# Optimization experiments

Measured on AMD Instinct MI355X. Metric: run time of the kernel, lower is better.

The kernel has to match this reference:

```python
import jax, jax.numpy as jnp
import numpy as np

B, S, D, H, FF, R, NB = 8, 1024, 768, 12, 3072, 16, 768


def _ln(x, g, b, eps=1e-6):
    m = x.mean(-1, keepdims=True)
    v = jnp.mean((x - m) ** 2, axis=-1, keepdims=True)
    return (x - m) * jax.lax.rsqrt(v + eps) * g + b


def setup_inputs() -> dict:
    key = jax.random.key(0)

    def rn(i, shape, s=0.02):
        return jax.random.normal(jax.random.fold_in(key, i), shape, jnp.float32) * s

    inp = {
        "x": jax.random.normal(jax.random.fold_in(key, 0), (B, S, D), jnp.float32),
        "attn_mask": jnp.zeros((S, S), jnp.float32),
        "norm1_g": jnp.ones((D,), jnp.float32),
        "norm1_b": jnp.zeros((D,), jnp.float32),
        "q_w": rn(1, (D, D)), "q_b": jnp.zeros((D,), jnp.float32),
        "k_w": rn(2, (D, D)), "k_b": jnp.zeros((D,), jnp.float32),
        "v_w": rn(3, (D, D)), "v_b": jnp.zeros((D,), jnp.float32),
        "o_w": rn(4, (D, D)), "o_b": jnp.zeros((D,), jnp.float32),
        "norm2_g": jnp.ones((D,), jnp.float32),
        "norm2_b": jnp.zeros((D,), jnp.float32),
        "fc1_w": rn(5, (FF, D)), "fc1_b": jnp.zeros((FF,), jnp.float32),
        "fc2_w": rn(6, (D, FF)), "fc2_b": jnp.zeros((D,), jnp.float32),
        # shared LoRA (backbone tokens)
        "lora1_A": rn(7, (D, R)), "lora1_B": rn(8, (R, FF)),
        "lora2_A": rn(9, (FF, R)), "lora2_B": rn(10, (R, D)),
        # expert VeRA: frozen shared A/B, per-expert diagonal scaling vectors
        "vera1_A": rn(11, (D, R)), "vera1_B": rn(12, (R, FF)),
        "vera2_A": rn(13, (FF, R)), "vera2_B": rn(14, (R, D)),
        "expert_fc1_d": rn(15, (R,), 1.0), "expert_fc1_b": rn(16, (FF,), 1.0),
        "expert_fc2_d": rn(17, (R,), 1.0), "expert_fc2_b": rn(18, (D,), 1.0),
        "num_backbone_tokens": NB,
    }
    return inp


def reference(x, attn_mask, norm1_g, norm1_b, q_w, q_b, k_w, k_b, v_w, v_b,
              o_w, o_b, norm2_g, norm2_b, fc1_w, fc1_b, fc2_w, fc2_b,
              lora1_A, lora1_B, lora2_A, lora2_B,
              vera1_A, vera1_B, vera2_A, vera2_B,
              expert_fc1_d, expert_fc1_b, expert_fc2_d, expert_fc2_b,
              num_backbone_tokens):
    bsz, seq, dim = x.shape
    hd = dim // H                      # head_dim = 64
    scale = hd ** -0.5
    nb = num_backbone_tokens

    # ---- attention (manual bmm + mask + softmax, eval-mode dropout = identity) ----
    h = _ln(x, norm1_g, norm1_b)
    q = (h @ q_w.T + q_b).reshape(bsz, seq, H, hd)
    k = (h @ k_w.T + k_b).reshape(bsz, seq, H, hd)
    v = (h @ v_w.T + v_b).reshape(bsz, seq, H, hd)
    scores = jnp.einsum('bqhd,bkhd->bhqk', q * scale, k) + attn_mask  # [B,H,S,S]
    probs = jax.nn.softmax(scores, axis=-1)
    ao = jnp.einsum('bhqk,bkhd->bqhd', probs, v).reshape(bsz, seq, dim)
    x = x + (ao @ o_w.T + o_b)

    # ---- MLP with split backbone (shared LoRA) / expert (VeRA) adapters ----
    residual = x
    n2 = _ln(x, norm2_g, norm2_b)
    hid = n2 @ fc1_w.T + fc1_b                                   # [B,S,FF]
    hid_b = hid[:, :nb] + (n2[:, :nb] @ lora1_A) @ lora1_B
    hid_e = hid[:, nb:] + (((n2[:, nb:] @ vera1_A) * expert_fc1_d) @ vera1_B) * expert_fc1_b
    hid = jnp.concatenate([hid_b, hid_e], axis=1)
    hid = jax.nn.gelu(hid)
    out = hid @ fc2_w.T + fc2_b                                  # [B,S,D]
    out_b = out[:, :nb] + (hid[:, :nb] @ lora2_A) @ lora2_B
    out_e = out[:, nb:] + (((hid[:, nb:] @ vera2_A) * expert_fc2_d) @ vera2_B) * expert_fc2_b
    out = jnp.concatenate([out_b, out_e], axis=1)
    return residual + out
```

## Files before the change

kernel.cpp:

```cpp
#include <hip/hip_runtime.h>
#include <stdint.h>

#define B_  8
#define S_  1024
#define D_  768
#define H_  12
#define HD_ 64
#define FF_ 3072
#define M_  (B_*S_)
#define R_  16
#define QLD 2304

typedef unsigned short u16;
typedef short s16x8 __attribute__((ext_vector_type(8)));
typedef float fx4  __attribute__((ext_vector_type(4)));

__device__ __forceinline__ float b2f(u16 u) {
  union { unsigned int i; float f; } c; c.i = ((unsigned int)u) << 16; return c.f;
}
__device__ __forceinline__ u16 f2b(float f) {
  union { float f; unsigned int i; } c; c.f = f;
  unsigned int x = c.i;
  x += 0x7FFFu + ((x >> 16) & 1u);
  return (u16)(x >> 16);
}
__device__ __forceinline__ float gelu_f(float x) {
  float u = 0.7978845608028654f * (x + 0.044715f * x * x * x);
  float e = __expf(2.f * u);
  float t = 1.f - 2.f / (e + 1.f);
  return 0.5f * x * (1.f + t);
}
__device__ __forceinline__ void gload16(const u16* gsrc, u16* ldst) {
  __builtin_amdgcn_global_load_lds(
      (__attribute__((address_space(1))) void*)(gsrc),
      (__attribute__((address_space(3))) void*)(ldst), 16, 0, 0);
}

__global__ __launch_bounds__(256)
void cvt_f2b(const float* __restrict__ in, u16* __restrict__ out, int n4) {
  const int i = blockIdx.x * 256 + threadIdx.x;
  if (i < n4) {
    const float4 f = ((const float4*)in)[i];
    ushort4 o4; o4.x = f2b(f.x); o4.y = f2b(f.y); o4.z = f2b(f.z); o4.w = f2b(f.w);
    ((ushort4*)out)[i] = o4;
  }
}

__global__ __launch_bounds__(256)
void prep_qkvb(const float* qb, const float* kb, const float* vb, float* out) {
  const int i = blockIdx.x * 256 + threadIdx.x;
  if (i < QLD) out[i] = (i < D_) ? qb[i] : (i < 2 * D_) ? kb[i - D_] : vb[i - 2 * D_];
}
__global__ __launch_bounds__(256)
void prep_up(const float* __restrict__ Blora, const float* __restrict__ Bvera,
             const float* __restrict__ evec, u16* __restrict__ upL,
             u16* __restrict__ upV, int N) {
  const int f = blockIdx.x * 256 + threadIdx.x;
  if (f >= N) return;
  const float ev = evec[f];
  #pragma unroll
  for (int r = 0; r < 16; ++r) {
    upL[(size_t)f * 32 + r] = f2b(Blora[(size_t)r * N + f]);
    upV[(size_t)f * 32 + r] = f2b(Bvera[(size_t)r * N + f] * ev);
    upL[(size_t)f * 32 + 16 + r] = 0;
    upV[(size_t)f * 32 + 16 + r] = 0;
  }
}
__global__ __launch_bounds__(256)
void prep_a2t(const float* __restrict__ Alora, const float* __restrict__ Avera,
              u16* __restrict__ tL, u16* __restrict__ tV) {
  const int f = blockIdx.x * 256 + threadIdx.x;
  if (f >= FF_) return;
  const float4* apl = (const float4*)(Alora + (size_t)f * 16);
  const float4* apv = (const float4*)(Avera + (size_t)f * 16);
  #pragma unroll
  for (int q4 = 0; q4 < 4; ++q4) {
    const float4 l4 = apl[q4], v4 = apv[q4];
    tL[(size_t)(q4 * 4 + 0) * FF_ + f] = f2b(l4.x);
    tL[(size_t)(q4 * 4 + 1) * FF_ + f] = f2b(l4.y);
    tL[(size_t)(q4 * 4 + 2) * FF_ + f] = f2b(l4.z);
    tL[(size_t)(q4 * 4 + 3) * FF_ + f] = f2b(l4.w);
    tV[(size_t)(q4 * 4 + 0) * FF_ + f] = f2b(v4.x);
    tV[(size_t)(q4 * 4 + 1) * FF_ + f] = f2b(v4.y);
    tV[(size_t)(q4 * 4 + 2) * FF_ + f] = f2b(v4.z);
    tV[(size_t)(q4 * 4 + 3) * FF_ + f] = f2b(v4.w);
  }
}

template<bool ADD>
__global__ __launch_bounds__(256)
void ln_k(const float* __restrict__ x, const u16* __restrict__ add,
          const float* __restrict__ g, const float* __restrict__ beta,
          u16* __restrict__ outb, float* __restrict__ xsum,
          const float* __restrict__ Alora, const float* __restrict__ Avera,
          const float* __restrict__ dvec, u16* __restrict__ tmp1b,
          const int* __restrict__ nbp)
{
  const int row = blockIdx.x;
  const size_t base = (size_t)row * D_;
  float v0[3]; float s = 0.f, sq = 0.f;
  #pragma unroll
  for (int i = 0; i < 3; ++i) {
    const int d = threadIdx.x + i * 256;
    float val = x[base + d];
    if (ADD) { val += b2f(add[base + d]); xsum[base + d] = val; }
    v0[i] = val; s += val; sq += val * val;
  }
  #pragma unroll
  for (int mm = 32; mm >= 1; mm >>= 1) { s += __shfl_xor(s, mm); sq += __shfl_xor(sq, mm); }
  __shared__ float ss[4], s2[4];
  if ((threadIdx.x & 63) == 0) { ss[threadIdx.x >> 6] = s; s2[threadIdx.x >> 6] = sq; }
  __syncthreads();
  s  = ss[0] + ss[1] + ss[2] + ss[3];
  sq = s2[0] + s2[1] + s2[2] + s2[3];
  const float mean = s * (1.f / D_);
  const float var  = sq * (1.f / D_) - mean * mean;
  const float rs   = rsqrtf(var + 1e-6f);
  float nv[3];
  #pragma unroll
  for (int i = 0; i < 3; ++i) {
    const int d = threadIdx.x + i * 256;
    nv[i] = (v0[i] - mean) * rs * g[d] + beta[d];
    outb[base + d] = f2b(nv[i]);
  }

  if (ADD) {
    const int nb = *nbp;
    const bool ex = (row % S_) >= nb;
    const float* Am = ex ? Avera : Alora;
    float p[16];
    #pragma unroll
    for (int r = 0; r < 16; ++r) p[r] = 0.f;
    #pragma unroll
    for (int i = 0; i < 3; ++i) {
      const int d = threadIdx.x + i * 256;
      const float4* ap = (const float4*)(Am + (size_t)d * R_);
      const float4 a0 = ap[0], a1 = ap[1], a2 = ap[2], a3 = ap[3];
      const float vv = nv[i];
      p[0]  += vv * a0.x; p[1]  += vv * a0.y; p[2]  += vv * a0.z; p[3]  += vv * a0.w;
      p[4]  += vv * a1.x; p[5]  += vv * a1.y; p[6]  += vv * a1.z; p[7]  += vv * a1.w;
      p[8]  += vv * a2.x; p[9]  += vv * a2.y; p[10] += vv * a2.z; p[11] += vv * a2.w;
      p[12] += vv * a3.x; p[13] += vv * a3.y; p[14] += vv * a3.z; p[15] += vv * a3.w;
    }
    #pragma unroll
    for (int st = 1; st < 16; st <<= 1)
      #pragma unroll
      for (int r = 0; r < 16; ++r) p[r] += __shfl_xor(p[r], st);
    __shared__ float sred[16][16];
    const int grp = threadIdx.x >> 4;
    if ((threadIdx.x & 15) == 0) {
      #pragma unroll
      for (int r = 0; r < 16; ++r) sred[grp][r] = p[r];
    }
    __syncthreads();
    if (threadIdx.x < 16) {
      float v = 0.f;
      #pragma unroll
      for (int gg = 0; gg < 16; ++gg) v += sred[gg][threadIdx.x];
      if (ex) v *= dvec[threadIdx.x];
      tmp1b[(size_t)row * 32 + threadIdx.x] = f2b(v);
      tmp1b[(size_t)row * 32 + 16 + threadIdx.x] = 0;
    }
  }
}

template<int MODE>
__global__ __launch_bounds__(256)
void gemm_bt(const u16* __restrict__ A, const u16* __restrict__ W,
             const float* __restrict__ bias, u16* __restrict__ Cb,
             float* __restrict__ Cf, const float* __restrict__ resid,
             const u16* __restrict__ Aad, const u16* __restrict__ BadL,
             const u16* __restrict__ BadV, const int* __restrict__ nbp,
             int M, int N, int K)
{
  __shared__ u16 As[128 * 32];
  __shared__ u16 Bs[128 * 32];
  const int tid   = threadIdx.x;
  const int lane  = tid & 63;
  const int wid   = tid >> 6;
  const int wr    = wid >> 1;
  const int wc    = wid & 1;
  const int lr    = lane & 15;
  const int lk    = (lane >> 4) << 3;
  const int m0    = blockIdx.x * 128;
  const int n0    = blockIdx.y * 128;
  const int kg    = (tid & 3) * 8;
  const int row_a = tid >> 2;

  fx4 acc[4][4];
  const fx4 zero = {0.f, 0.f, 0.f, 0.f};
  #pragma unroll
  for (int i = 0; i < 4; ++i)
    #pragma unroll
    for (int j = 0; j < 4; ++j) acc[i][j] = zero;

  for (int k0 = 0; k0 < K; k0 += 32) {
    #pragma unroll
    for (int u = 0; u < 2; ++u) {
      const int row = u * 64 + row_a;
      const int li  = u * 256 + tid;
      gload16(A + (size_t)(m0 + row) * K + k0 + kg, &As[li * 8]);
      gload16(W + (size_t)(n0 + row) * K + k0 + kg, &Bs[li * 8]);
    }
    __syncthreads();
    s16x8 av[4], bv[4];
    #pragma unroll
    for (int i = 0; i < 4; ++i)
      av[i] = *(const s16x8*)&As[(wr * 64 + i * 16 + lr) * 32 + lk];
    #pragma unroll
    for (int j = 0; j < 4; ++j)
      bv[j] = *(const s16x8*)&Bs[(wc * 64 + j * 16 + lr) * 32 + lk];
    #pragma unroll
    for (int i = 0; i < 4; ++i)
      #pragma unroll
      for (int j = 0; j < 4; ++j)
        acc[i][j] = __builtin_amdgcn_mfma_f32_16x16x32_bf16(av[i], bv[j], acc[i][j], 0, 0, 0);
    __syncthreads();
  }

  if (MODE >= 1) {
    const int nb = *nbp;
    const u16* Bad = ((m0 % S_) >= nb) ? BadV : BadL;
    #pragma unroll
    for (int u = 0; u < 2; ++u) {
      const int row = u * 64 + row_a;
      const int li  = u * 256 + tid;
      gload16(Aad + (size_t)(m0 + row) * 32 + kg, &As[li * 8]);
      gload16(Bad + (size_t)(n0 + row) * 32 + kg, &Bs[li * 8]);
    }
    __syncthreads();
    s16x8 av[4], bv[4];
    #pragma unroll
    for (int i = 0; i < 4; ++i)
      av[i] = *(const s16x8*)&As[(wr * 64 + i * 16 + lr) * 32 + lk];
    #pragma unroll
    for (int j = 0; j < 4; ++j)
      bv[j] = *(const s16x8*)&Bs[(wc * 64 + j * 16 + lr) * 32 + lk];
    #pragma unroll
    for (int i = 0; i < 4; ++i)
      #pragma unroll
      for (int j = 0; j < 4; ++j)
        acc[i][j] = __builtin_amdgcn_mfma_f32_16x16x32_bf16(av[i], bv[j], acc[i][j], 0, 0, 0);
    __syncthreads();
  }

  const int rb = (lane >> 4) * 4;
  #pragma unroll
  for (int j = 0; j < 4; ++j) {
    const int col = n0 + wc * 64 + j * 16 + lr;
    const float bj = bias ? bias[col] : 0.f;
    #pragma unroll
    for (int i = 0; i < 4; ++i) {
      const int row = m0 + wr * 64 + i * 16 + rb;
      #pragma unroll
      for (int r = 0; r < 4; ++r) {
        const float val = acc[i][j][r] + bj;
        const size_t idx = (size_t)(row + r) * N + col;
        if (MODE == 1)      Cb[idx] = f2b(gelu_f(val));
        else if (MODE == 2) Cf[idx] = resid[idx] + val;
        else                Cb[idx] = f2b(val);
      }
    }
  }
}

__global__ __launch_bounds__(256)
void downproj(const u16* __restrict__ hid, const u16* __restrict__ A2tL,
              const u16* __restrict__ A2tV, float* __restrict__ part,
              const int* __restrict__ nbp)
{
  __shared__ u16 As[128 * 32];
  __shared__ u16 Bs[16 * 32];
  const int tid  = threadIdx.x;
  const int lane = tid & 63;
  const int w    = tid >> 6;
  const int lr   = lane & 15;
  const int lk   = (lane >> 4) << 3;
  const int m0   = blockIdx.x * 128;
  const int kb   = blockIdx.y * (FF_ / 8);
  const int nb   = *nbp;
  const u16* A2t = ((m0 % S_) >= nb) ? A2tV : A2tL;
  const int kg    = (tid & 3) * 8;
  const int row_a = tid >> 2;

  const fx4 zero = {0.f, 0.f, 0.f, 0.f};
  fx4 acc[2]; acc[0] = zero; acc[1] = zero;

  for (int k0 = kb; k0 < kb + FF_ / 8; k0 += 32) {
    #pragma unroll
    for (int u = 0; u < 2; ++u)
      gload16(hid + (size_t)(m0 + u * 64 + row_a) * FF_ + k0 + kg,
              &As[(u * 256 + tid) * 8]);
    if (tid < 64)
      gload16(A2t + (size_t)(tid >> 2) * FF_ + k0 + kg, &Bs[tid * 8]);
    __syncthreads();
    s16x8 bv = *(const s16x8*)&Bs[lr * 32 + lk];
    #pragma unroll
    for (int i = 0; i < 2; ++i) {
      s16x8 av = *(const s16x8*)&As[(w * 32 + i * 16 + lr) * 32 + lk];
      acc[i] = __builtin_amdgcn_mfma_f32_16x16x32_bf16(av, bv, acc[i], 0, 0, 0);
    }
    __syncthreads();
  }

  const int rb = (lane >> 4) * 4;
  #pragma unroll
  for (int i = 0; i < 2; ++i)
    #pragma unroll
    for (int r = 0; r < 4; ++r)
      part[(size_t)blockIdx.y * M_ * 16 +
           (size_t)(m0 + w * 32 + i * 16 + rb + r) * 16 + lr] = acc[i][r];
}

__global__ __launch_bounds__(256)
void reduce_dp(const float* __restrict__ part, const float* __restrict__ d2,
               u16* __restrict__ tmp2b, const int* __restrict__ nbp)
{
  const int idx = blockIdx.x * 256 + threadIdx.x;
  const int m = idx >> 4, r = idx & 15;
  const int nb = *nbp;
  float s = 0.f;
  #pragma unroll
  for (int ks = 0; ks < 8; ++ks) s += part[(size_t)ks * M_ * 16 + idx];
  if ((m % S_) >= nb) s *= d2[r];
  tmp2b[(size_t)m * 32 + r] = f2b(s);
  tmp2b[(size_t)m * 32 + 16 + r] = 0;
}

__global__ __launch_bounds__(256)
void attn_mfma(const u16* __restrict__ qkv, const float* __restrict__ mask,
               u16* __restrict__ o)
{
  __shared__ u16 Ql[64 * 64];
  __shared__ u16 Kl[64 * 64];
  __shared__ u16 Vt[64 * 64];
  __shared__ u16 Pl[4][16 * 64];

  const int tid  = threadIdx.x;
  const int lane = tid & 63;
  const int wq   = tid >> 6;
  const int lr   = lane & 15;
  const int hi   = lane >> 4;
  const int qb   = blockIdx.x;
  const int bh   = blockIdx.y;
  const int b    = bh / H_;
  const int h    = bh % H_;
  const size_t tok0 = (size_t)b * S_ + (size_t)qb * 64;
  const size_t colh = (size_t)h * HD_;

  #pragma unroll
  for (int u = 0; u < 2; ++u) {
    const int li = u * 256 + tid;
    const int r  = li >> 3;
    const int cb = ((li & 7) ^ (r & 7)) * 8;
    gload16(qkv + (tok0 + r) * QLD + colh + cb, &Ql[li * 8]);
  }
  __syncthreads();

  s16x8 qa[2];
  {
    const int qrow = wq * 16 + lr;
    #pragma unroll
    for (int ks = 0; ks < 2; ++ks)
      qa[ks] = *(const s16x8*)&Ql[qrow * 64 + ((ks * 32 + hi * 8) ^ ((qrow & 7) << 3))];
  }

  const fx4 zero = {0.f, 0.f, 0.f, 0.f};
  fx4 oacc[4];
  #pragma unroll
  for (int dj = 0; dj < 4; ++dj) oacc[dj] = zero;
  float mreg[4], lreg[4];
  #pragma unroll
  for (int r = 0; r < 4; ++r) { mreg[r] = -3.0e38f; lreg[r] = 0.f; }

  for (int kt = 0; kt < S_ / 64; ++kt) {
    const size_t ktok = (size_t)b * S_ + (size_t)kt * 64;
    __syncthreads();

    #pragma unroll
    for (int u = 0; u < 2; ++u) {
      const int li = u * 256 + tid;
      const int r  = li >> 3;
      const int cb = ((li & 7) ^ (r & 7)) * 8;
      gload16(qkv + (ktok + r) * QLD + D_ + colh + cb, &Kl[li * 8]);
    }
    {
      const int a  = tid >> 3;
      const int c8 = (tid & 7) * 8;
      const u16* vp = qkv + (ktok + 2 * a) * QLD + 2 * D_ + colh + c8;
      s16x8 v0 = *(const s16x8*)vp;
      s16x8 v1 = *(const s16x8*)(vp + QLD);
      #pragma unroll
      for (int jj = 0; jj < 8; ++jj) {
        const int d  = c8 + jj;
        const int sw = ((d & 7) ^ ((d >> 3) & 7)) << 3;
        const int cp = (2 * a) ^ sw;
        *(uint32_t*)&Vt[d * 64 + cp] =
            (uint32_t)(u16)v0[jj] | ((uint32_t)(u16)v1[jj] << 16);
      }
    }
    __syncthreads();

    float mv[4][4];
    {
      const float* mp = mask + (size_t)(qb * 64 + wq * 16 + hi * 4) * S_ + (size_t)kt * 64 + lr;
      #pragma unroll
      for (int r = 0; r < 4; ++r)
        #pragma unroll
        for (int j = 0; j < 4; ++j)
          mv[j][r] = mp[(size_t)r * S_ + j * 16];
    }

    s16x8 kb2[4][2];
    #pragma unroll
    for (int j = 0; j < 4; ++j) {
      const int n = j * 16 + lr;
      #pragma unroll
      for (int ks = 0; ks < 2; ++ks)
        kb2[j][ks] = *(const s16x8*)&Kl[n * 64 + ((ks * 32 + hi * 8) ^ ((n & 7) << 3))];
    }
    fx4 sf[4];
    #pragma unroll
    for (int j = 0; j < 4; ++j) sf[j] = zero;
    #pragma unroll
    for (int ks = 0; ks < 2; ++ks)
      #pragma unroll
      for (int j = 0; j < 4; ++j)
        sf[j] = __builtin_amdgcn_mfma_f32_16x16x32_bf16(qa[ks], kb2[j][ks], sf[j], 0, 0, 0);

    float val[4][4];
    #pragma unroll
    for (int j = 0; j < 4; ++j)
      #pragma unroll
      for (int r = 0; r < 4; ++r)
        val[j][r] = sf[j][r] * 0.125f + mv[j][r];
    #pragma unroll
    for (int r = 0; r < 4; ++r) {
      float mx = fmaxf(fmaxf(val[0][r], val[1][r]), fmaxf(val[2][r], val[3][r]));
      mx = fmaxf(mx, __shfl_xor(mx, 1));
      mx = fmaxf(mx, __shfl_xor(mx, 2));
      mx = fmaxf(mx, __shfl_xor(mx, 4));
      mx = fmaxf(mx, __shfl_xor(mx, 8));
      const float mn  = fmaxf(mreg[r], mx);
      const float fac = __expf(mreg[r] - mn);
      mreg[r] = mn;
      float rs = 0.f;
      #pragma unroll
      for (int j = 0; j < 4; ++j) {
        const float p = __expf(val[j][r] - mn);
        val[j][r] = p;
        rs += p;
      }
      rs += __shfl_xor(rs, 1); rs += __shfl_xor(rs, 2);
      rs += __shfl_xor(rs, 4); rs += __shfl_xor(rs, 8);
      lreg[r] = lreg[r] * fac + rs;
      #pragma unroll
      for (int dj = 0; dj < 4; ++dj) oacc[dj][r] *= fac;
    }

    #pragma unroll
    for (int j = 0; j < 4; ++j) {
      const int col = j * 16 + lr;
      #pragma unroll
      for (int r = 0; r < 4; ++r) {
        const int row = hi * 4 + r;
        Pl[wq][row * 64 + (col ^ ((row & 7) << 3))] = f2b(val[j][r]);
      }
    }
    s16x8 pa[2];
    #pragma unroll
    for (int ks = 0; ks < 2; ++ks)
      pa[ks] = *(const s16x8*)&Pl[wq][lr * 64 + ((ks * 32 + hi * 8) ^ ((lr & 7) << 3))];

    s16x8 bv2[4][2];
    #pragma unroll
    for (int dj = 0; dj < 4; ++dj) {
      const int n  = dj * 16 + lr;
      const int sw = ((n & 7) ^ ((n >> 3) & 7)) << 3;
      #pragma unroll
      for (int ks = 0; ks < 2; ++ks)
        bv2[dj][ks] = *(const s16x8*)&Vt[n * 64 + ((ks * 32 + hi * 8) ^ sw)];
    }
    #pragma unroll
    for (int ks = 0; ks < 2; ++ks)
      #pragma unroll
      for (int dj = 0; dj < 4; ++dj)
        oacc[dj] = __builtin_amdgcn_mfma_f32_16x16x32_bf16(pa[ks], bv2[dj][ks], oacc[dj], 0, 0, 0);
  }

  #pragma unroll
  for (int r = 0; r < 4; ++r) {
    const float inv = 1.f / lreg[r];
    const size_t grow = (tok0 + wq * 16 + hi * 4 + r) * D_ + colh;
    #pragma unroll
    for (int dj = 0; dj < 4; ++dj)
      o[grow + dj * 16 + lr] = f2b(oacc[dj][r] * inv);
  }
}

extern "C" void kernel_launch(void* const* d_in, const int* in_sizes, int n_in,
                              void* d_out, int out_size, void* d_ws, size_t ws_size,
                              hipStream_t stream)
{
  const float* x      = (const float*)d_in[0];
  const float* mask   = (const float*)d_in[1];
  const float* n1g    = (const float*)d_in[2];
  const float* n1b    = (const float*)d_in[3];
  const float* q_w    = (const float*)d_in[4];
  const float* q_bv   = (const float*)d_in[5];
  const float* k_w    = (const float*)d_in[6];
  const float* k_bv   = (const float*)d_in[7];
  const float* v_w    = (const float*)d_in[8];
  const float* v_bv   = (const float*)d_in[9];
  const float* o_w    = (const float*)d_in[10];
  const float* o_bv   = (const float*)d_in[11];
  const float* n2g    = (const float*)d_in[12];
  const float* n2b    = (const float*)d_in[13];
  const float* fc1_w  = (const float*)d_in[14];
  const float* fc1_bv = (const float*)d_in[15];
  const float* fc2_w  = (const float*)d_in[16];
  const float* fc2_bv = (const float*)d_in[17];
  const float* lora1A = (const float*)d_in[18];
  const float* lora1B = (const float*)d_in[19];
  const float* lora2A = (const float*)d_in[20];
  const float* lora2B = (const float*)d_in[21];
  const float* vera1A = (const float*)d_in[22];
  const float* vera1B = (const float*)d_in[23];
  const float* vera2A = (const float*)d_in[24];
  const float* vera2B = (const float*)d_in[25];
  const float* e1d    = (const float*)d_in[26];
  const float* e1b    = (const float*)d_in[27];
  const float* e2d    = (const float*)d_in[28];
  const float* e2b    = (const float*)d_in[29];
  const int*   nbp    = (const int*)d_in[30];

  char* wsb = (char*)d_ws;
  u16* h1    = (u16*)wsb; wsb += (size_t)M_ * D_ * 2;
  u16* qkv   = (u16*)wsb; wsb += (size_t)M_ * QLD * 2;
  u16* attno = (u16*)wsb; wsb += (size_t)M_ * D_ * 2;
  u16* oproj = (u16*)wsb; wsb += (size_t)M_ * D_ * 2;
  u16* n2    = (u16*)wsb; wsb += (size_t)M_ * D_ * 2;
  u16* wqkv  = (u16*)wsb; wsb += (size_t)QLD * D_ * 2;
  u16* wo    = (u16*)wsb; wsb += (size_t)D_ * D_ * 2;
  u16* wfc1  = (u16*)wsb; wsb += (size_t)FF_ * D_ * 2;
  u16* wfc2  = (u16*)wsb; wsb += (size_t)D_ * FF_ * 2;
  u16* tmp1b = (u16*)wsb; wsb += (size_t)M_ * 32 * 2;
  u16* tmp2b = (u16*)wsb; wsb += (size_t)M_ * 32 * 2;
  u16* up1L  = (u16*)wsb; wsb += (size_t)FF_ * 32 * 2;
  u16* up1V  = (u16*)wsb; wsb += (size_t)FF_ * 32 * 2;
  u16* up2L  = (u16*)wsb; wsb += (size_t)D_ * 32 * 2;
  u16* up2V  = (u16*)wsb; wsb += (size_t)D_ * 32 * 2;
  u16* a2tL  = (u16*)wsb; wsb += (size_t)16 * FF_ * 2;
  u16* a2tV  = (u16*)wsb; wsb += (size_t)16 * FF_ * 2;
  float* qkvb = (float*)wsb; wsb += (size_t)QLD * 4;
  float* part = (float*)wsb; wsb += (size_t)8 * M_ * 16 * 4;
  u16* hidb = h1;

  cvt_f2b<<<(D_*D_/4 + 255)/256, 256, 0, stream>>>(q_w, wqkv,              D_*D_/4);
  cvt_f2b<<<(D_*D_/4 + 255)/256, 256, 0, stream>>>(k_w, wqkv +   D_*D_,    D_*D_/4);
  cvt_f2b<<<(D_*D_/4 + 255)/256, 256, 0, stream>>>(v_w, wqkv + 2*D_*D_,    D_*D_/4);
  cvt_f2b<<<(D_*D_/4 + 255)/256, 256, 0, stream>>>(o_w,   wo,   D_*D_/4);
  cvt_f2b<<<(FF_*D_/4 + 255)/256, 256, 0, stream>>>(fc1_w, wfc1, FF_*D_/4);
  cvt_f2b<<<(D_*FF_/4 + 255)/256, 256, 0, stream>>>(fc2_w, wfc2, D_*FF_/4);
  prep_qkvb<<<(QLD + 255)/256, 256, 0, stream>>>(q_bv, k_bv, v_bv, qkvb);
  prep_up<<<(FF_ + 255)/256, 256, 0, stream>>>(lora1B, vera1B, e1b, up1L, up1V, FF_);
  prep_up<<<(D_  + 255)/256, 256, 0, stream>>>(lora2B, vera2B, e2b, up2L, up2V, D_);
  prep_a2t<<<(FF_ + 255)/256, 256, 0, stream>>>(lora2A, vera2A, a2tL, a2tV);

  ln_k<false><<<M_, 256, 0, stream>>>(x, nullptr, n1g, n1b, h1, nullptr,
                                      nullptr, nullptr, nullptr, nullptr, nullptr);
  gemm_bt<0><<<dim3(M_/128, QLD/128), 256, 0, stream>>>(
      h1, wqkv, qkvb, qkv, nullptr, nullptr, nullptr, nullptr, nullptr, nullptr,
      M_, QLD, D_);
  attn_mfma<<<dim3(S_/64, B_*H_), 256, 0, stream>>>(qkv, mask, attno);
  gemm_bt<0><<<dim3(M_/128, D_/128), 256, 0, stream>>>(
      attno, wo, o_bv, oproj, nullptr, nullptr, nullptr, nullptr, nullptr, nullptr,
      M_, D_, D_);

  ln_k<true><<<M_, 256, 0, stream>>>(x, oproj, n2g, n2b, n2, (float*)d_out,
                                     lora1A, vera1A, e1d, tmp1b, nbp);

  gemm_bt<1><<<dim3(M_/128, FF_/128), 256, 0, stream>>>(
      n2, wfc1, fc1_bv, hidb, nullptr, nullptr, tmp1b, up1L, up1V, nbp,
      M_, FF_, D_);

  downproj<<<dim3(M_/128, 8), 256, 0, stream>>>(hidb, a2tL, a2tV, part, nbp);
  reduce_dp<<<M_*16/256, 256, 0, stream>>>(part, e2d, tmp2b, nbp);

  gemm_bt<2><<<dim3(M_/128, D_/128), 256, 0, stream>>>(
      hidb, wfc2, fc2_bv, nullptr, (float*)d_out, (const float*)d_out,
      tmp2b, up2L, up2V, nbp, M_, D_, FF_);
}
```

Before: 403.5 us.

## Widen attention key tile to 128 and merge weight-prep launches

The attention kernel now processes 128 keys per iteration instead of 64. This halves the number of loop trips and barriers, and it reuses the Q buffer's shared memory for the P tiles. MFMA sections are wrapped in s_setprio so other waves can keep issuing loads while the matrix units work. The six weight conversions are merged into one kernel and the four small prep kernels into another, cutting launch count. The trade-offs are more LDS and register use per block, which may lower occupancy, plus extra branching in the merged prep kernels.

Measured after the change: 385.8 us. 1.05x faster.

```diff
diff --git a/kernel.cpp b/kernel.cpp
--- a/kernel.cpp
+++ b/kernel.cpp
@@ -10,6 +10,7 @@
 #define M_  (B_*S_)
 #define R_  16
 #define QLD 2304
+#define KBLK 128
 
 typedef unsigned short u16;
 typedef short s16x8 __attribute__((ext_vector_type(8)));
@@ -37,53 +38,75 @@
 }
 
 __global__ __launch_bounds__(256)
-void cvt_f2b(const float* __restrict__ in, u16* __restrict__ out, int n4) {
+void cvt_all(const float* __restrict__ q_w, const float* __restrict__ k_w,
+             const float* __restrict__ v_w, const float* __restrict__ o_w,
+             const float* __restrict__ fc1_w, const float* __restrict__ fc2_w,
+             u16* __restrict__ wqkv, u16* __restrict__ wo,
+             u16* __restrict__ wfc1, u16* __restrict__ wfc2)
+{
   const int i = blockIdx.x * 256 + threadIdx.x;
-  if (i < n4) {
-    const float4 f = ((const float4*)in)[i];
-    ushort4 o4; o4.x = f2b(f.x); o4.y = f2b(f.y); o4.z = f2b(f.z); o4.w = f2b(f.w);
-    ((ushort4*)out)[i] = o4;
-  }
+  const int q1  = D_ * D_ / 4;
+  const int fd4 = FF_ * D_ / 4;
+  const float* s; u16* d; int j;
+  if      (i <     q1)       { s = q_w;   d = wqkv;            j = i; }
+  else if (i < 2 * q1)       { s = k_w;   d = wqkv + D_*D_;    j = i - q1; }
+  else if (i < 3 * q1)       { s = v_w;   d = wqkv + 2*D_*D_;  j = i - 2*q1; }
+  else if (i < 4 * q1)       { s = o_w;   d = wo;              j = i - 3*q1; }
+  else if (i < 4 * q1 + fd4) { s = fc1_w; d = wfc1;            j = i - 4*q1; }
+  else                       { s = fc2_w; d = wfc2;            j = i - 4*q1 - fd4; }
+  const float4 f = ((const float4*)s)[j];
+  ushort4 o4; o4.x = f2b(f.x); o4.y = f2b(f.y); o4.z = f2b(f.z); o4.w = f2b(f.w);
+  ((ushort4*)d)[j] = o4;
 }
 
 __global__ __launch_bounds__(256)
-void prep_qkvb(const float* qb, const float* kb, const float* vb, float* out) {
-  const int i = blockIdx.x * 256 + threadIdx.x;
-  if (i < QLD) out[i] = (i < D_) ? qb[i] : (i < 2 * D_) ? kb[i - D_] : vb[i - 2 * D_];
-}
-__global__ __launch_bounds__(256)
-void prep_up(const float* __restrict__ Blora, const float* __restrict__ Bvera,
-             const float* __restrict__ evec, u16* __restrict__ upL,
-             u16* __restrict__ upV, int N) {
+void prep_all(const float* __restrict__ q_bv, const float* __restrict__ k_bv,
+              const float* __restrict__ v_bv, float* __restrict__ qkvb,
+              const float* __restrict__ lora1B, const float* __restrict__ vera1B,
+              const float* __restrict__ e1b, u16* __restrict__ up1L, u16* __restrict__ up1V,
+              const float* __restrict__ lora2B, const float* __restrict__ vera2B,
+              const float* __restrict__ e2b, u16* __restrict__ up2L, u16* __restrict__ up2V,
+              const float* __restrict__ lora2A, const float* __restrict__ vera2A,
+              u16* __restrict__ a2tL, u16* __restrict__ a2tV)
+{
   const int f = blockIdx.x * 256 + threadIdx.x;
-  if (f >= N) return;
-  const float ev = evec[f];
-  #pragma unroll
-  for (int r = 0; r < 16; ++r) {
-    upL[(size_t)f * 32 + r] = f2b(Blora[(size_t)r * N + f]);
-    upV[(size_t)f * 32 + r] = f2b(Bvera[(size_t)r * N + f] * ev);
-    upL[(size_t)f * 32 + 16 + r] = 0;
-    upV[(size_t)f * 32 + 16 + r] = 0;
-  }
-}
-__global__ __launch_bounds__(256)
-void prep_a2t(const float* __restrict__ Alora, const float* __restrict__ Avera,
-              u16* __restrict__ tL, u16* __restrict__ tV) {
-  const int f = blockIdx.x * 256 + threadIdx.x;
-  if (f >= FF_) return;
-  const float4* apl = (const float4*)(Alora + (size_t)f * 16);
-  const float4* apv = (const float4*)(Avera + (size_t)f * 16);
-  #pragma unroll
-  for (int q4 = 0; q4 < 4; ++q4) {
-    const float4 l4 = apl[q4], v4 = apv[q4];
-    tL[(size_t)(q4 * 4 + 0) * FF_ + f] = f2b(l4.x);
-    tL[(size_t)(q4 * 4 + 1) * FF_ + f] = f2b(l4.y);
-    tL[(size_t)(q4 * 4 + 2) * FF_ + f] = f2b(l4.z);
-    tL[(size_t)(q4 * 4 + 3) * FF_ + f] = f2b(l4.w);
-    tV[(size_t)(q4 * 4 + 0) * FF_ + f] = f2b(v4.x);
-    tV[(size_t)(q4 * 4 + 1) * FF_ + f] = f2b(v4.y);
-    tV[(size_t)(q4 * 4 + 2) * FF_ + f] = f2b(v4.z);
-    tV[(size_t)(q4 * 4 + 3) * FF_ + f] = f2b(v4.w);
+  if (f < QLD)
+    qkvb[f] = (f < D_) ? q_bv[f] : (f < 2 * D_) ? k_bv[f - D_] : v_bv[f - 2 * D_];
+  {
+    const float ev = e1b[f];
+    #pragma unroll
+    for (int r = 0; r < 16; ++r) {
+      up1L[(size_t)f * 32 + r] = f2b(lora1B[(size_t)r * FF_ + f]);
+      up1V[(size_t)f * 32 + r] = f2b(vera1B[(size_t)r * FF_ + f] * ev);
+      up1L[(size_t)f * 32 + 16 + r] = 0;
+      up1V[(size_t)f * 32 + 16 + r] = 0;
+    }
+  }
+  {
+    const float4* apl = (const float4*)(lora2A + (size_t)f * 16);
+    const float4* apv = (const float4*)(vera2A + (size_t)f * 16);
+    #pragma unroll
+    for (int q4 = 0; q4 < 4; ++q4) {
+      const float4 l4 = apl[q4], v4 = apv[q4];
+      a2tL[(size_t)(q4*4+0) * FF_ + f] = f2b(l4.x);
+      a2tL[(size_t)(q4*4+1) * FF_ + f] = f2b(l4.y);
+      a2tL[(size_t)(q4*4+2) * FF_ + f] = f2b(l4.z);
+      a2tL[(size_t)(q4*4+3) * FF_ + f] = f2b(l4.w);
+      a2tV[(size_t)(q4*4+0) * FF_ + f] = f2b(v4.x);
+      a2tV[(size_t)(q4*4+1) * FF_ + f] = f2b(v4.y);
+      a2tV[(size_t)(q4*4+2) * FF_ + f] = f2b(v4.z);
+      a2tV[(size_t)(q4*4+3) * FF_ + f] = f2b(v4.w);
+    }
+  }
+  if (f < D_) {
+    const float ev = e2b[f];
+    #pragma unroll
+    for (int r = 0; r < 16; ++r) {
+      up2L[(size_t)f * 32 + r] = f2b(lora2B[(size_t)r * D_ + f]);
+      up2V[(size_t)f * 32 + r] = f2b(vera2B[(size_t)r * D_ + f] * ev);
+      up2L[(size_t)f * 32 + 16 + r] = 0;
+      up2V[(size_t)f * 32 + 16 + r] = 0;
+    }
   }
 }
 
@@ -331,10 +354,9 @@
 void attn_mfma(const u16* __restrict__ qkv, const float* __restrict__ mask,
                u16* __restrict__ o)
 {
-  __shared__ u16 Ql[64 * 64];
-  __shared__ u16 Kl[64 * 64];
-  __shared__ u16 Vt[64 * 64];
-  __shared__ u16 Pl[4][16 * 64];
+  __shared__ u16 Kl[128 * 64];
+  __shared__ u16 Vt[64 * 128];
+  __shared__ u16 QP[4 * 2048];
 
   const int tid  = threadIdx.x;
   const int lane = tid & 63;
@@ -353,16 +375,15 @@
     const int li = u * 256 + tid;
     const int r  = li >> 3;
     const int cb = ((li & 7) ^ (r & 7)) * 8;
-    gload16(qkv + (tok0 + r) * QLD + colh + cb, &Ql[li * 8]);
+    gload16(qkv + (tok0 + r) * QLD + colh + cb, &QP[li * 8]);
   }
   __syncthreads();
-
   s16x8 qa[2];
   {
     const int qrow = wq * 16 + lr;
     #pragma unroll
     for (int ks = 0; ks < 2; ++ks)
-      qa[ks] = *(const s16x8*)&Ql[qrow * 64 + ((ks * 32 + hi * 8) ^ ((qrow & 7) << 3))];
+      qa[ks] = *(const s16x8*)&QP[qrow * 64 + ((ks * 32 + hi * 8) ^ ((qrow & 7) << 3))];
   }
 
   const fx4 zero = {0.f, 0.f, 0.f, 0.f};
@@ -373,12 +394,12 @@
   #pragma unroll
   for (int r = 0; r < 4; ++r) { mreg[r] = -3.0e38f; lreg[r] = 0.f; }
 
-  for (int kt = 0; kt < S_ / 64; ++kt) {
-    const size_t ktok = (size_t)b * S_ + (size_t)kt * 64;
-    __syncthreads();
-
-    #pragma unroll
-    for (int u = 0; u < 2; ++u) {
+  for (int kt = 0; kt < S_ / KBLK; ++kt) {
+    const size_t ktok = (size_t)b * S_ + (size_t)kt * KBLK;
+    __syncthreads();
+
+    #pragma unroll
+    for (int u = 0; u < 4; ++u) {
       const int li = u * 256 + tid;
       const int r  = li >> 3;
       const int cb = ((li & 7) ^ (r & 7)) * 8;
@@ -387,56 +408,67 @@
     {
       const int a  = tid >> 3;
       const int c8 = (tid & 7) * 8;
-      const u16* vp = qkv + (ktok + 2 * a) * QLD + 2 * D_ + colh + c8;
+      const u16* vp = qkv + (ktok + 4 * a) * QLD + 2 * D_ + colh + c8;
       s16x8 v0 = *(const s16x8*)vp;
       s16x8 v1 = *(const s16x8*)(vp + QLD);
+      s16x8 v2 = *(const s16x8*)(vp + 2 * QLD);
+      s16x8 v3 = *(const s16x8*)(vp + 3 * QLD);
       #pragma unroll
       for (int jj = 0; jj < 8; ++jj) {
         const int d  = c8 + jj;
         const int sw = ((d & 7) ^ ((d >> 3) & 7)) << 3;
-        const int cp = (2 * a) ^ sw;
-        *(uint32_t*)&Vt[d * 64 + cp] =
+        const int cp = (4 * a) ^ sw;
+        *(uint32_t*)&Vt[d * 128 + cp] =
             (uint32_t)(u16)v0[jj] | ((uint32_t)(u16)v1[jj] << 16);
+        *(uint32_t*)&Vt[d * 128 + cp + 2] =
+            (uint32_t)(u16)v2[jj] | ((uint32_t)(u16)v3[jj] << 16);
       }
     }
     __syncthreads();
 
-    float mv[4][4];
-    {
-      const float* mp = mask + (size_t)(qb * 64 + wq * 16 + hi * 4) * S_ + (size_t)kt * 64 + lr;
-      #pragma unroll
-      for (int r = 0; r < 4; ++r)
+    float val[8][4];
+    #pragma unroll
+    for (int jh = 0; jh < 2; ++jh) {
+      s16x8 kb2[4][2];
+      #pragma unroll
+      for (int j = 0; j < 4; ++j) {
+        const int n = (jh * 4 + j) * 16 + lr;
+        #pragma unroll
+        for (int ks = 0; ks < 2; ++ks)
+          kb2[j][ks] = *(const s16x8*)&Kl[n * 64 + ((ks * 32 + hi * 8) ^ ((n & 7) << 3))];
+      }
+      float mvh[4][4];
+      {
+        const float* mp = mask + (size_t)(qb * 64 + wq * 16 + hi * 4) * S_
+                        + (size_t)kt * KBLK + jh * 64 + lr;
         #pragma unroll
         for (int j = 0; j < 4; ++j)
-          mv[j][r] = mp[(size_t)r * S_ + j * 16];
-    }
-
-    s16x8 kb2[4][2];
-    #pragma unroll
-    for (int j = 0; j < 4; ++j) {
-      const int n = j * 16 + lr;
+          #pragma unroll
+          for (int r = 0; r < 4; ++r)
+            mvh[j][r] = mp[(size_t)r * S_ + j * 16];
+      }
+      fx4 sf[4];
+      #pragma unroll
+      for (int j = 0; j < 4; ++j) sf[j] = zero;
+      __builtin_amdgcn_s_setprio(1);
       #pragma unroll
       for (int ks = 0; ks < 2; ++ks)
-        kb2[j][ks] = *(const s16x8*)&Kl[n * 64 + ((ks * 32 + hi * 8) ^ ((n & 7) << 3))];
-    }
-    fx4 sf[4];
-    #pragma unroll
-    for (int j = 0; j < 4; ++j) sf[j] = zero;
-    #pragma unroll
-    for (int ks = 0; ks < 2; ++ks)
+        #pragma unroll
+        for (int j = 0; j < 4; ++j)
+          sf[j] = __builtin_amdgcn_mfma_f32_16x16x32_bf16(qa[ks], kb2[j][ks], sf[j], 0, 0, 0);
+      __builtin_amdgcn_s_setprio(0);
       #pragma unroll
       for (int j = 0; j < 4; ++j)
-        sf[j] = __builtin_amdgcn_mfma_f32_16x16x32_bf16(qa[ks], kb2[j][ks], sf[j], 0, 0, 0);
-
-    float val[4][4];
-    #pragma unroll
-    for (int j = 0; j < 4; ++j)
-      #pragma unroll
-      for (int r = 0; r < 4; ++r)
-        val[j][r] = sf[j][r] * 0.125f + mv[j][r];
+        #pragma unroll
+        for (int r = 0; r < 4; ++r)
+          val[jh * 4 + j][r] = sf[j][r] * 0.125f + mvh[j][r];
+    }
+
     #pragma unroll
     for (int r = 0; r < 4; ++r) {
-      float mx = fmaxf(fmaxf(val[0][r], val[1][r]), fmaxf(val[2][r], val[3][r]));
+      float mx = val[0][r];
+      #pragma unroll
+      for (int j = 1; j < 8; ++j) mx = fmaxf(mx, val[j][r]);
       mx = fmaxf(mx, __shfl_xor(mx, 1));
       mx = fmaxf(mx, __shfl_xor(mx, 2));
       mx = fmaxf(mx, __shfl_xor(mx, 4));
@@ -446,7 +478,7 @@
       mreg[r] = mn;
       float rs = 0.f;
       #pragma unroll
-      for (int j = 0; j < 4; ++j) {
+      for (int j = 0; j < 8; ++j) {
         const float p = __expf(val[j][r] - mn);
         val[j][r] = p;
         rs += p;
@@ -459,33 +491,32 @@
     }
 
     #pragma unroll
-    for (int j = 0; j < 4; ++j) {
+    for (int j = 0; j < 8; ++j) {
       const int col = j * 16 + lr;
       #pragma unroll
       for (int r = 0; r < 4; ++r) {
         const int row = hi * 4 + r;
-        Pl[wq][row * 64 + (col ^ ((row & 7) << 3))] = f2b(val[j][r]);
+        QP[wq * 2048 + row * 128 + (col ^ ((row & 7) << 3))] = f2b(val[j][r]);
       }
     }
-    s16x8 pa[2];
-    #pragma unroll
-    for (int ks = 0; ks < 2; ++ks)
-      pa[ks] = *(const s16x8*)&Pl[wq][lr * 64 + ((ks * 32 + hi * 8) ^ ((lr & 7) << 3))];
-
-    s16x8 bv2[4][2];
-    #pragma unroll
-    for (int dj = 0; dj < 4; ++dj) {
-      const int n  = dj * 16 + lr;
-      const int sw = ((n & 7) ^ ((n >> 3) & 7)) << 3;
-      #pragma unroll
-      for (int ks = 0; ks < 2; ++ks)
-        bv2[dj][ks] = *(const s16x8*)&Vt[n * 64 + ((ks * 32 + hi * 8) ^ sw)];
-    }
-    #pragma unroll
-    for (int ks = 0; ks < 2; ++ks)
+
+    #pragma unroll
+    for (int ks = 0; ks < 4; ++ks) {
+      s16x8 pa = *(const s16x8*)&QP[wq * 2048 + lr * 128 +
+                                    ((ks * 32 + hi * 8) ^ ((lr & 7) << 3))];
+      s16x8 bv2[4];
+      #pragma unroll
+      for (int dj = 0; dj < 4; ++dj) {
+        const int n  = dj * 16 + lr;
+        const int sw = ((n & 7) ^ ((n >> 3) & 7)) << 3;
+        bv2[dj] = *(const s16x8*)&Vt[n * 128 + ((ks * 32 + hi * 8) ^ sw)];
+      }
+      __builtin_amdgcn_s_setprio(1);
       #pragma unroll
       for (int dj = 0; dj < 4; ++dj)
-        oacc[dj] = __builtin_amdgcn_mfma_f32_16x16x32_bf16(pa[ks], bv2[dj][ks], oacc[dj], 0, 0, 0);
+        oacc[dj] = __builtin_amdgcn_mfma_f32_16x16x32_bf16(pa, bv2[dj], oacc[dj], 0, 0, 0);
+      __builtin_amdgcn_s_setprio(0);
+    }
   }
 
   #pragma unroll
@@ -556,16 +587,13 @@
   float* part = (float*)wsb; wsb += (size_t)8 * M_ * 16 * 4;
   u16* hidb = h1;
 
-  cvt_f2b<<<(D_*D_/4 + 255)/256, 256, 0, stream>>>(q_w, wqkv,              D_*D_/4);
-  cvt_f2b<<<(D_*D_/4 + 255)/256, 256, 0, stream>>>(k_w, wqkv +   D_*D_,    D_*D_/4);
-  cvt_f2b<<<(D_*D_/4 + 255)/256, 256, 0, stream>>>(v_w, wqkv + 2*D_*D_,    D_*D_/4);
-  cvt_f2b<<<(D_*D_/4 + 255)/256, 256, 0, stream>>>(o_w,   wo,   D_*D_/4);
-  cvt_f2b<<<(FF_*D_/4 + 255)/256, 256, 0, stream>>>(fc1_w, wfc1, FF_*D_/4);
-  cvt_f2b<<<(D_*FF_/4 + 255)/256, 256, 0, stream>>>(fc2_w, wfc2, D_*FF_/4);
-  prep_qkvb<<<(QLD + 255)/256, 256, 0, stream>>>(q_bv, k_bv, v_bv, qkvb);
-  prep_up<<<(FF_ + 255)/256, 256, 0, stream>>>(lora1B, vera1B, e1b, up1L, up1V, FF_);
-  prep_up<<<(D_  + 255)/256, 256, 0, stream>>>(lora2B, vera2B, e2b, up2L, up2V, D_);
-  prep_a2t<<<(FF_ + 255)/256, 256, 0, stream>>>(lora2A, vera2A, a2tL, a2tV);
+  const int totq = (4 * D_ * D_ + 2 * FF_ * D_) / 4;
+  cvt_all<<<totq / 256, 256, 0, stream>>>(q_w, k_w, v_w, o_w, fc1_w, fc2_w,
+                                          wqkv, wo, wfc1, wfc2);
+  prep_all<<<FF_ / 256, 256, 0, stream>>>(q_bv, k_bv, v_bv, qkvb,
+                                          lora1B, vera1B, e1b, up1L, up1V,
+                                          lora2B, vera2B, e2b, up2L, up2V,
+                                          lora2A, vera2A, a2tL, a2tV);
 
   ln_k<false><<<M_, 256, 0, stream>>>(x, nullptr, n1g, n1b, h1, nullptr,
                                       nullptr, nullptr, nullptr, nullptr, nullptr);
```
